# Optimization experiments

Hardware: AMD Instinct MI355X
Metric: run time of the kernel (lower is better)

The kernel has to match this reference:

```python
import jax, jax.numpy as jnp
import numpy as np
from jax import lax

D_MODEL = 1024
D_STATE = 16
D_CONV = 4
EXPAND = 2
D_INNER = EXPAND * D_MODEL            # 2048
DT_RANK = (D_MODEL + 15) // 16        # 64
B, L = 2, 2048
EPS = 1e-5


def setup_inputs() -> dict:
    key = jax.random.key(0)
    ks = jax.random.split(key, 12)
    s = 0.02
    x = jax.random.normal(ks[0], (B, L, D_MODEL), dtype=jnp.float32)
    norm_w = jnp.ones((D_MODEL,), dtype=jnp.float32)
    in_proj_w = jax.random.normal(ks[1], (2 * D_INNER, D_MODEL), dtype=jnp.float32) * s
    conv_w = jax.random.normal(ks[2], (D_INNER, D_CONV), dtype=jnp.float32) * 0.1
    conv_b = jax.random.normal(ks[3], (D_INNER,), dtype=jnp.float32) * 0.01
    x_proj_w = jax.random.normal(ks[4], (DT_RANK + 2 * D_STATE, D_INNER), dtype=jnp.float32) * s
    dt_proj_w = jax.random.normal(ks[5], (D_INNER, DT_RANK), dtype=jnp.float32) * 0.1
    dt_proj_b = jax.random.normal(ks[6], (D_INNER,), dtype=jnp.float32) * 0.5 - 4.0  # small softplus(delta)
    # S4D-real init: A = -(1..d_state) per channel
    A_log = jnp.log(jnp.broadcast_to(jnp.arange(1, D_STATE + 1, dtype=jnp.float32), (D_INNER, D_STATE)))
    Dp = jnp.ones((D_INNER,), dtype=jnp.float32)
    out_proj_w = jax.random.normal(ks[7], (D_MODEL, D_INNER), dtype=jnp.float32) * s
    return {"x": x, "norm_w": norm_w, "in_proj_w": in_proj_w, "conv_w": conv_w,
            "conv_b": conv_b, "x_proj_w": x_proj_w, "dt_proj_w": dt_proj_w,
            "dt_proj_b": dt_proj_b, "A_log": A_log, "Dp": Dp, "out_proj_w": out_proj_w}


def _selective_scan(deltaA, deltaBu, Cm):
    # deltaA, deltaBu: [B,L,Di,N]; Cm: [B,L,N] -> y: [B,L,Di]
    def step(h, inp):
        dA, dBu, c = inp
        h = dA * h + dBu                       # [B,Di,N]
        y = jnp.einsum('bdn,bn->bd', h, c)     # [B,Di]
        return h, y
    h0 = jnp.zeros(deltaA.shape[0:1] + deltaA.shape[2:], deltaA.dtype)
    _, ys = lax.scan(step, h0, (deltaA.transpose(1, 0, 2, 3),
                                deltaBu.transpose(1, 0, 2, 3),
                                Cm.transpose(1, 0, 2)))
    return ys.transpose(1, 0, 2)               # [B,L,Di]


def reference(x, norm_w, in_proj_w, conv_w, conv_b, x_proj_w,
              dt_proj_w, dt_proj_b, A_log, Dp, out_proj_w):
    d_inner, d_conv = conv_w.shape
    d_state = A_log.shape[1]
    dt_rank = dt_proj_w.shape[1]

    # RMSNorm
    rms = jnp.sqrt(jnp.mean(x * x, axis=-1, keepdims=True) + EPS)
    xn = norm_w * (x / rms)

    # input projection -> x, z streams
    xz = jnp.einsum('bld,ed->ble', xn, in_proj_w)      # [B,L,2*Di]
    xi, z = jnp.split(xz, 2, axis=-1)

    # depthwise causal conv1d + SiLU
    xc = lax.conv_general_dilated(
        xi.transpose(0, 2, 1), conv_w[:, None, :], (1,), [(d_conv - 1, 0)],
        dimension_numbers=('NCL', 'OIL', 'NCL'), feature_group_count=d_inner)
    xc = jax.nn.silu(xc.transpose(0, 2, 1) + conv_b)   # [B,L,Di]

    # input-dependent SSM params
    dbl = jnp.einsum('bld,ed->ble', xc, x_proj_w)      # [B,L,dt_rank+2N]
    dt, Bm, Cm = jnp.split(dbl, [dt_rank, dt_rank + d_state], axis=-1)
    delta = jax.nn.softplus(jnp.einsum('blr,dr->bld', dt, dt_proj_w) + dt_proj_b)

    A = -jnp.exp(A_log)                                # [Di,N]
    deltaA = jnp.exp(delta[..., None] * A)             # [B,L,Di,N]
    deltaBu = delta[..., None] * Bm[:, :, None, :] * xc[..., None]

    y = _selective_scan(deltaA, deltaBu, Cm)           # [B,L,Di]
    y = y + xc * Dp
    y = y * jax.nn.silu(z)

    out = jnp.einsum('bld,ed->ble', y, out_proj_w)     # [B,L,d_model]
    return x + out
```

## Files before the change

### kernel.cpp

```cpp
#include <hip/hip_runtime.h>
#include <hip/hip_bf16.h>
#include <math.h>

#define D_MODEL 1024
#define D_STATE 16
#define D_CONV 4
#define D_INNER 2048
#define DT_RANK 64
#define BATCH 2
#define SEQ 2048
#define NTOK (BATCH*SEQ)
#define EPS 1e-5f
#define CCH 32
#define TCH (SEQ/CCH)
#define XKS 8
#define XKC (D_INNER/XKS)

typedef __attribute__((ext_vector_type(8))) short short8;
typedef __attribute__((ext_vector_type(4))) float f32x4;
typedef __attribute__((ext_vector_type(4))) unsigned short us4;

__device__ inline unsigned short f2bf(float f) {
  union { __hip_bfloat16 h; unsigned short u; } c;
  c.h = __float2bfloat16(f);
  return c.u;
}
__device__ inline float bf2f(unsigned short u) {
  union { unsigned int i; float f; } c;
  c.i = ((unsigned int)u) << 16;
  return c.f;
}

#define GLL(gp, lp) __builtin_amdgcn_global_load_lds( \
    (const __attribute__((address_space(1))) void*)(gp), \
    (__attribute__((address_space(3))) void*)(lp), 16, 0, 0)

__global__ __launch_bounds__(256) void f2bf4_kernel(
    const float* __restrict__ i0, unsigned short* __restrict__ o0, int b0,
    const float* __restrict__ i1, unsigned short* __restrict__ o1, int b1,
    const float* __restrict__ i2, unsigned short* __restrict__ o2, int b2,
    const float* __restrict__ i3, unsigned short* __restrict__ o3)
{
  int blk = blockIdx.x;
  const float* in; unsigned short* out; int base;
  if (blk < b0)           { in = i0; out = o0; base = blk; }
  else if (blk < b0+b1)   { in = i1; out = o1; base = blk - b0; }
  else if (blk < b0+b1+b2){ in = i2; out = o2; base = blk - b0 - b1; }
  else                    { in = i3; out = o3; base = blk - b0 - b1 - b2; }
  int i = (base*256 + threadIdx.x)*4;
  float4 v = *(const float4*)(in + i);
  us4 o;
  o[0] = f2bf(v.x); o[1] = f2bf(v.y); o[2] = f2bf(v.z); o[3] = f2bf(v.w);
  *(us4*)(out + i) = o;
}

__global__ __launch_bounds__(256) void rmsnorm_kernel(const float* __restrict__ x,
                                                      const float* __restrict__ w,
                                                      unsigned short* __restrict__ xn) {
  int tok = blockIdx.x;
  const float* xr = x + (size_t)tok * D_MODEL;
  unsigned short* xo = xn + (size_t)tok * D_MODEL;
  int t = threadIdx.x;
  float4 v = ((const float4*)xr)[t];
  float ss = v.x*v.x + v.y*v.y + v.z*v.z + v.w*v.w;
  #pragma unroll
  for (int off = 32; off > 0; off >>= 1) ss += __shfl_down(ss, off, 64);
  __shared__ float wsum[4];
  __shared__ float rinv_s;
  int lane = t & 63, wv = t >> 6;
  if (lane == 0) wsum[wv] = ss;
  __syncthreads();
  if (t == 0) {
    float tot = wsum[0] + wsum[1] + wsum[2] + wsum[3];
    rinv_s = 1.0f / sqrtf(tot / (float)D_MODEL + EPS);
  }
  __syncthreads();
  float rinv = rinv_s;
  float4 g = ((const float4*)w)[t];
  us4 o;
  o[0] = f2bf(v.x * rinv * g.x);
  o[1] = f2bf(v.y * rinv * g.y);
  o[2] = f2bf(v.z * rinv * g.z);
  o[3] = f2bf(v.w * rinv * g.w);
  *(us4*)(xo + t*4) = o;
}

template<int EPI, int OBF>
__global__ __launch_bounds__(256) void gemm_bf16_kernel(
    const unsigned short* __restrict__ A,
    const unsigned short* __restrict__ W,
    void* __restrict__ Cv, int ldc, int K,
    const float* __restrict__ bias,
    const float* __restrict__ resid)
{
  __shared__ __align__(16) unsigned short Abuf[8*64*8];
  __shared__ __align__(16) unsigned short Bbuf[8*64*8];
  int tid = threadIdx.x;
  int lane = tid & 63;
  int w = tid >> 6;
  int bm = blockIdx.x * 128;
  int bn = blockIdx.y * 128;
  int wrow = (w >> 1) * 64;
  int wcol = (w & 1) * 64;

  int r15 = lane & 15, g = lane >> 4;
  const unsigned short* Ag0 = A + (size_t)(bm + 2*w*16 + r15) * K + g*8;
  const unsigned short* Ag1 = Ag0 + (size_t)16 * K;
  const unsigned short* Wg0 = W + (size_t)(bn + 2*w*16 + r15) * K + g*8;
  const unsigned short* Wg1 = Wg0 + (size_t)16 * K;
  unsigned short* Al0 = &Abuf[(2*w  )*512];
  unsigned short* Al1 = &Abuf[(2*w+1)*512];
  unsigned short* Bl0 = &Bbuf[(2*w  )*512];
  unsigned short* Bl1 = &Bbuf[(2*w+1)*512];

  f32x4 acc[4][4] = {};

  for (int k0 = 0; k0 < K; k0 += 32) {
    __syncthreads();
    GLL(Ag0 + k0, Al0);
    GLL(Ag1 + k0, Al1);
    GLL(Wg0 + k0, Bl0);
    GLL(Wg1 + k0, Bl1);
    __syncthreads();

    short8 af[4], bfr[4];
    #pragma unroll
    for (int i = 0; i < 4; ++i)
      af[i] = *(const short8*)&Abuf[((wrow >> 4) + i)*512 + lane*8];
    #pragma unroll
    for (int j = 0; j < 4; ++j)
      bfr[j] = *(const short8*)&Bbuf[((wcol >> 4) + j)*512 + lane*8];
    #pragma unroll
    for (int i = 0; i < 4; ++i)
      #pragma unroll
      for (int j = 0; j < 4; ++j)
        acc[i][j] = __builtin_amdgcn_mfma_f32_16x16x32_bf16(af[i], bfr[j], acc[i][j], 0, 0, 0);
  }

  #pragma unroll
  for (int i = 0; i < 4; ++i) {
    #pragma unroll
    for (int j = 0; j < 4; ++j) {
      #pragma unroll
      for (int r = 0; r < 4; ++r) {
        int row = bm + wrow + i*16 + (lane >> 4)*4 + r;
        int col = bn + wcol + j*16 + (lane & 15);
        float v = acc[i][j][r];
        if (EPI == 1) {
          float s = v + bias[col];
          v = fmaxf(s, 0.f) + log1pf(__expf(-fabsf(s)));
        } else if (EPI == 2) {
          v += resid[(size_t)row * ldc + col];
        }
        if (OBF) ((unsigned short*)Cv)[(size_t)row * ldc + col] = f2bf(v);
        else     ((float*)Cv)[(size_t)row * ldc + col] = v;
      }
    }
  }
}

__global__ __launch_bounds__(256) void xproj_bf16_kernel(
    const unsigned short* __restrict__ A,
    const unsigned short* __restrict__ W,
    float* __restrict__ Ppart)
{
  __shared__ __align__(16) unsigned short Abuf[8*512];
  __shared__ __align__(16) unsigned short Bbuf[6*512];
  int tid = threadIdx.x;
  int lane = tid & 63;
  int w = tid >> 6;
  int bm = blockIdx.x * 128;
  int kc = blockIdx.y;
  const int K = D_INNER;
  int r15 = lane & 15, g = lane >> 4;

  const unsigned short* Ag0 = A + (size_t)(bm + 2*w*16 + r15) * K + g*8 + kc*XKC;
  const unsigned short* Ag1 = Ag0 + (size_t)16 * K;
  const unsigned short* Wg0 = W + (size_t)(w*16 + r15) * K + g*8 + kc*XKC;
  const unsigned short* Wg1 = W + (size_t)((4+w)*16 + r15) * K + g*8 + kc*XKC;
  unsigned short* Al0 = &Abuf[(2*w  )*512];
  unsigned short* Al1 = &Abuf[(2*w+1)*512];
  unsigned short* Bl0 = &Bbuf[w*512];
  unsigned short* Bl1 = &Bbuf[(4+w)*512];

  f32x4 acc[2][6] = {};

  for (int k0 = 0; k0 < XKC; k0 += 32) {
    __syncthreads();
    GLL(Ag0 + k0, Al0);
    GLL(Ag1 + k0, Al1);
    GLL(Wg0 + k0, Bl0);
    if (w < 2) GLL(Wg1 + k0, Bl1);
    __syncthreads();

    short8 af[2], bfr[6];
    #pragma unroll
    for (int i = 0; i < 2; ++i)
      af[i] = *(const short8*)&Abuf[(2*w + i)*512 + lane*8];
    #pragma unroll
    for (int j = 0; j < 6; ++j)
      bfr[j] = *(const short8*)&Bbuf[j*512 + lane*8];
    #pragma unroll
    for (int i = 0; i < 2; ++i)
      #pragma unroll
      for (int j = 0; j < 6; ++j)
        acc[i][j] = __builtin_amdgcn_mfma_f32_16x16x32_bf16(af[i], bfr[j], acc[i][j], 0, 0, 0);
  }

  float* out = Ppart + (size_t)kc * NTOK * 96;
  #pragma unroll
  for (int i = 0; i < 2; ++i) {
    #pragma unroll
    for (int j = 0; j < 6; ++j) {
      #pragma unroll
      for (int r = 0; r < 4; ++r) {
        int row = bm + w*32 + i*16 + (lane >> 4)*4 + r;
        int col = j*16 + (lane & 15);
        out[(size_t)row * 96 + col] = acc[i][j][r];
      }
    }
  }
}

__global__ __launch_bounds__(256) void xproj_reduce_kernel(
    const float* __restrict__ Ppart, float* __restrict__ dbl,
    unsigned short* __restrict__ dtbf)
{
  int idx = blockIdx.x * 256 + threadIdx.x;
  float s = 0.f;
  #pragma unroll
  for (int k = 0; k < XKS; ++k) s += Ppart[(size_t)k * NTOK * 96 + idx];
  dbl[idx] = s;
  int row = idx / 96, col = idx - row * 96;
  if (col < DT_RANK) dtbf[(size_t)row * DT_RANK + col] = f2bf(s);
}

__global__ __launch_bounds__(256) void conv_silu_kernel(
    const unsigned short* __restrict__ xz, const float* __restrict__ cw,
    const float* __restrict__ cb, unsigned short* __restrict__ xcbf)
{
  int idx = blockIdx.x * 256 + threadIdx.x;
  int dq = idx & (D_INNER/4 - 1);
  int tok = idx >> 9;
  int l = tok & (SEQ - 1);
  int d = dq * 4;
  const unsigned short* xi = xz + (size_t)tok * (2*D_INNER) + d;
  us4 v3 = *(const us4*)xi;
  us4 v2 = l >= 1 ? *(const us4*)(xi - 1*(2*D_INNER)) : (us4)0;
  us4 v1 = l >= 2 ? *(const us4*)(xi - 2*(2*D_INNER)) : (us4)0;
  us4 v0 = l >= 3 ? *(const us4*)(xi - 3*(2*D_INNER)) : (us4)0;
  float4 cbv = *(const float4*)(cb + d);
  float cbx[4] = {cbv.x, cbv.y, cbv.z, cbv.w};
  us4 o;
  #pragma unroll
  for (int j = 0; j < 4; ++j) {
    float4 wv = *(const float4*)(cw + (d + j) * 4);
    float s = cbx[j];
    s = fmaf(bf2f(v0[j]), wv.x, s);
    s = fmaf(bf2f(v1[j]), wv.y, s);
    s = fmaf(bf2f(v2[j]), wv.z, s);
    s = fmaf(bf2f(v3[j]), wv.w, s);
    float v = s / (1.f + __expf(-s));
    o[j] = f2bf(v);
  }
  *(us4*)(xcbf + (size_t)tok * D_INNER + d) = o;
}

__global__ __launch_bounds__(256) void scan_pass1(
    const unsigned short* __restrict__ delta, const float* __restrict__ dbl,
    const unsigned short* __restrict__ xc, const float* __restrict__ A_log,
    float* __restrict__ P, float* __restrict__ He)
{
  int blk = blockIdx.x;
  int d = (blk & 7) * 256 + threadIdx.x;
  int c = (blk >> 3) & (CCH - 1);
  int b = blk >> 8;
  float Adn[16];
  #pragma unroll
  for (int n = 0; n < 16; ++n) Adn[n] = -__expf(A_log[d*16 + n]);
  float h[16] = {};
  float sdl = 0.f;
  int tok0 = b * SEQ + c * TCH;
  for (int t = 0; t < TCH; ++t) {
    size_t tok = (size_t)(tok0 + t);
    float dl = bf2f(delta[tok * D_INNER + d]);
    float xcv = bf2f(xc[tok * D_INNER + d]);
    float u = dl * xcv;
    const float4* bp = (const float4*)(dbl + tok*96 + 64);
    float4 b0 = bp[0], b1 = bp[1], b2 = bp[2], b3 = bp[3];
    float bv[16] = {b0.x,b0.y,b0.z,b0.w, b1.x,b1.y,b1.z,b1.w,
                    b2.x,b2.y,b2.z,b2.w, b3.x,b3.y,b3.z,b3.w};
    sdl += dl;
    #pragma unroll
    for (int n = 0; n < 16; ++n)
      h[n] = fmaf(__expf(dl * Adn[n]), h[n], u * bv[n]);
  }
  size_t base = ((size_t)(b*CCH + c) * 16) * D_INNER + d;
  #pragma unroll
  for (int n = 0; n < 16; ++n) {
    P [base + (size_t)n * D_INNER] = __expf(Adn[n] * sdl);
    He[base + (size_t)n * D_INNER] = h[n];
  }
}

__global__ __launch_bounds__(256) void scan_pass2(
    const float* __restrict__ P, const float* __restrict__ He,
    float* __restrict__ Hin)
{
  int blk = blockIdx.x;
  int d = (blk & 7) * 256 + threadIdx.x;
  int n = (blk >> 3) & 15;
  int b = blk >> 7;
  float h = 0.f;
  #pragma unroll 4
  for (int c = 0; c < CCH; ++c) {
    size_t idx = ((size_t)(b*CCH + c) * 16 + n) * D_INNER + d;
    Hin[idx] = h;
    h = fmaf(P[idx], h, He[idx]);
  }
}

__global__ __launch_bounds__(256) void scan_pass3(
    const unsigned short* __restrict__ delta, const float* __restrict__ dbl,
    const unsigned short* __restrict__ xc, const unsigned short* __restrict__ xz,
    const float* __restrict__ A_log, const float* __restrict__ Dp,
    const float* __restrict__ Hin, unsigned short* __restrict__ y)
{
  int blk = blockIdx.x;
  int d = (blk & 7) * 256 + threadIdx.x;
  int c = (blk >> 3) & (CCH - 1);
  int b = blk >> 8;
  float Adn[16];
  #pragma unroll
  for (int n = 0; n < 16; ++n) Adn[n] = -__expf(A_log[d*16 + n]);
  float Dpd = Dp[d];
  float h[16];
  size_t base = ((size_t)(b*CCH + c) * 16) * D_INNER + d;
  #pragma unroll
  for (int n = 0; n < 16; ++n) h[n] = Hin[base + (size_t)n * D_INNER];
  int tok0 = b * SEQ + c * TCH;
  for (int t = 0; t < TCH; ++t) {
    size_t tok = (size_t)(tok0 + t);
    float dl = bf2f(delta[tok * D_INNER + d]);
    float xcv = bf2f(xc[tok * D_INNER + d]);
    float u = dl * xcv;
    const float4* bp = (const float4*)(dbl + tok*96 + 64);
    float4 b0 = bp[0], b1 = bp[1], b2 = bp[2], b3 = bp[3];
    float4 c0 = bp[4], c1 = bp[5], c2 = bp[6], c3 = bp[7];
    float bv[16] = {b0.x,b0.y,b0.z,b0.w, b1.x,b1.y,b1.z,b1.w,
                    b2.x,b2.y,b2.z,b2.w, b3.x,b3.y,b3.z,b3.w};
    float cv[16] = {c0.x,c0.y,c0.z,c0.w, c1.x,c1.y,c1.z,c1.w,
                    c2.x,c2.y,c2.z,c2.w, c3.x,c3.y,c3.z,c3.w};
    float z = bf2f(xz[tok * (2*D_INNER) + D_INNER + d]);
    float acc = xcv * Dpd;
    #pragma unroll
    for (int n = 0; n < 16; ++n) {
      h[n] = fmaf(__expf(dl * Adn[n]), h[n], u * bv[n]);
      acc = fmaf(h[n], cv[n], acc);
    }
    float sz = z / (1.f + __expf(-z));
    y[tok * D_INNER + d] = f2bf(acc * sz);
  }
}

extern "C" void kernel_launch(void* const* d_in, const int* in_sizes, int n_in,
                              void* d_out, int out_size, void* d_ws, size_t ws_size,
                              hipStream_t stream) {
  const float* x         = (const float*)d_in[0];
  const float* norm_w    = (const float*)d_in[1];
  const float* in_proj_w = (const float*)d_in[2];
  const float* conv_w    = (const float*)d_in[3];
  const float* conv_b    = (const float*)d_in[4];
  const float* x_proj_w  = (const float*)d_in[5];
  const float* dt_proj_w = (const float*)d_in[6];
  const float* dt_proj_b = (const float*)d_in[7];
  const float* A_log     = (const float*)d_in[8];
  const float* Dp        = (const float*)d_in[9];
  const float* out_proj_w= (const float*)d_in[10];
  float* out = (float*)d_out;

  char* ws = (char*)d_ws;
  unsigned short* xz_bf   = (unsigned short*)(ws);
  unsigned short* xc_bf   = (unsigned short*)(ws + ( 32ull<<20));
  float*          dbl     = (float*)(ws + ( 48ull<<20));
  unsigned short* delta_bf= (unsigned short*)(ws + ( 50ull<<20));
  unsigned short* xn_bf   = (unsigned short*)(ws + ( 66ull<<20));
  unsigned short* w_in_bf = (unsigned short*)(ws + ( 74ull<<20));
  unsigned short* w_out_bf= (unsigned short*)(ws + ( 82ull<<20));
  unsigned short* w_xp_bf = (unsigned short*)(ws + ( 86ull<<20));
  unsigned short* w_dt_bf = (unsigned short*)(ws + ( 87ull<<20));
  unsigned short* dtbf    = (unsigned short*)(ws + ( 88ull<<20));
  float*          Ppart   = (float*)(ws + ( 89ull<<20));
  float*          Pst     = (float*)(ws + (102ull<<20));
  float*          Hest    = (float*)(ws + (110ull<<20));
  float*          Hin     = (float*)(ws + (118ull<<20));
  unsigned short* yb_bf   = (unsigned short*)(ws + (126ull<<20));

  rmsnorm_kernel<<<NTOK, 256, 0, stream>>>(x, norm_w, xn_bf);

  f2bf4_kernel<<<4096+2048+192+128, 256, 0, stream>>>(
      in_proj_w, w_in_bf, 4096,
      out_proj_w, w_out_bf, 2048,
      x_proj_w, w_xp_bf, 192,
      dt_proj_w, w_dt_bf);

  {
    dim3 g(NTOK/128, (2*D_INNER)/128);
    gemm_bf16_kernel<0,1><<<g, 256, 0, stream>>>(xn_bf, w_in_bf, xz_bf, 2*D_INNER, D_MODEL,
                                                 nullptr, nullptr);
  }

  conv_silu_kernel<<<(NTOK*D_INNER/4)/256, 256, 0, stream>>>(xz_bf, conv_w, conv_b, xc_bf);

  {
    dim3 g(NTOK/128, XKS);
    xproj_bf16_kernel<<<g, 256, 0, stream>>>(xc_bf, w_xp_bf, Ppart);
    xproj_reduce_kernel<<<(NTOK*96)/256, 256, 0, stream>>>(Ppart, dbl, dtbf);
  }

  {
    dim3 g(NTOK/128, D_INNER/128);
    gemm_bf16_kernel<1,1><<<g, 256, 0, stream>>>(dtbf, w_dt_bf, delta_bf, D_INNER, DT_RANK,
                                                 dt_proj_b, nullptr);
  }

  scan_pass1<<<BATCH*CCH*8, 256, 0, stream>>>(delta_bf, dbl, xc_bf, A_log, Pst, Hest);
  scan_pass2<<<BATCH*16*8, 256, 0, stream>>>(Pst, Hest, Hin);
  scan_pass3<<<BATCH*CCH*8, 256, 0, stream>>>(delta_bf, dbl, xc_bf, xz_bf, A_log, Dp, Hin, yb_bf);

  {
    dim3 g(NTOK/128, D_MODEL/128);
    gemm_bf16_kernel<2,0><<<g, 256, 0, stream>>>(yb_bf, w_out_bf, out, D_MODEL, D_INNER,
                                                 nullptr, x);
  }
}
```

Before: 385.3 us.

## Add 256x256 double-buffered MFMA GEMM kernel for in_proj

Replaces the 128x128 tile GEMM for the input projection with a new 512-thread kernel using 256x256 tiles. It loads global memory directly into LDS with double buffering and runs a four-phase software pipeline that interleaves MFMA with staged loads, controlled by explicit waitcnt, barriers and priority hints. The larger tiles raise data reuse per byte loaded. In exchange the grid shrinks to 256 blocks, LDS use rises to 128KB per block, and register pressure goes up, which limits occupancy.

```diff
diff --git a/kernel.cpp b/kernel.cpp
--- a/kernel.cpp
+++ b/kernel.cpp
@@ -83,6 +83,125 @@
   o[2] = f2bf(v.z * rinv * g.z);
   o[3] = f2bf(v.w * rinv * g.w);
   *(us4*)(xo + t*4) = o;
+}
+
+template<int NT>
+__global__ __launch_bounds__(512) void gemm256_bf16_kernel(
+    const unsigned short* __restrict__ A,
+    const unsigned short* __restrict__ W,
+    unsigned short* __restrict__ C, int ldc)
+{
+  const int K = NT*64;
+  __shared__ __align__(16) unsigned short As[2][16384];
+  __shared__ __align__(16) unsigned short Bs[2][16384];
+  int tid = threadIdx.x;
+  int lane = tid & 63;
+  int w = tid >> 6;
+  int wm = w >> 2, wn = w & 3;
+  int bm = blockIdx.x * 256;
+  int bn = blockIdx.y * 256;
+  int r15 = lane & 15, g8 = (lane >> 4) * 8;
+  int rbh0 = (w & 3) + (w >> 2) * 8;
+  int rbh1 = rbh0 + 4;
+
+  auto stageA = [&](int slot, int tile, int ks, int rb) {
+    const unsigned short* src = A + (size_t)(bm + rb*16 + r15) * K + tile*64 + ks*32 + g8;
+    GLL(src, &As[slot][rb*1024 + ks*512]);
+  };
+  auto stageB = [&](int slot, int tile, int ks, int cb) {
+    const unsigned short* src = W + (size_t)(bn + cb*16 + r15) * K + tile*64 + ks*32 + g8;
+    GLL(src, &Bs[slot][cb*1024 + ks*512]);
+  };
+
+  stageA(0,0,0,rbh0); stageB(0,0,0,w); stageB(0,0,0,8+w);
+  stageA(0,0,0,rbh1);
+  stageA(0,0,1,rbh0); stageB(0,0,1,w); stageB(0,0,1,8+w);
+  stageA(0,0,1,rbh1);
+  stageA(1,1,0,rbh0); stageB(1,1,0,w); stageB(1,1,0,8+w);
+  stageA(1,1,0,rbh1);
+  stageA(1,1,1,rbh0); stageB(1,1,1,w); stageB(1,1,1,8+w);
+  asm volatile("s_waitcnt vmcnt(7)" ::: "memory");
+  __builtin_amdgcn_s_barrier();
+  __builtin_amdgcn_sched_barrier(0);
+
+  f32x4 acc[8][4] = {};
+  short8 bfr[4];
+
+#define PHASE_END()                                                      \
+  if (drain) { asm volatile("s_waitcnt vmcnt(0)" ::: "memory"); }        \
+  else       { asm volatile("s_waitcnt vmcnt(12)" ::: "memory"); }       \
+  __builtin_amdgcn_s_barrier();                                          \
+  __builtin_amdgcn_sched_barrier(0);
+
+#define MFMA16(IH)                                                       \
+  __builtin_amdgcn_s_setprio(1);                                         \
+  _Pragma("unroll")                                                      \
+  for (int ii = 0; ii < 4; ++ii) {                                       \
+    _Pragma("unroll")                                                    \
+    for (int j = 0; j < 4; ++j)                                          \
+      acc[(IH)*4+ii][j] = __builtin_amdgcn_mfma_f32_16x16x32_bf16(       \
+          af[ii], bfr[j], acc[(IH)*4+ii][j], 0, 0, 0);                   \
+  }                                                                      \
+  __builtin_amdgcn_s_setprio(0);
+
+#define LOAD_A(KS, IH)                                                   \
+  short8 af[4];                                                          \
+  _Pragma("unroll")                                                      \
+  for (int ii = 0; ii < 4; ++ii)                                         \
+    af[ii] = *(const short8*)&As[s][(wm*8 + (IH)*4 + ii)*1024 + (KS)*512 + lane*8];
+
+#define LOAD_B(KS)                                                       \
+  _Pragma("unroll")                                                      \
+  for (int j = 0; j < 4; ++j)                                            \
+    bfr[j] = *(const short8*)&Bs[s][(wn*4 + j)*1024 + (KS)*512 + lane*8];
+
+  for (int t = 0; t < NT; ++t) {
+    int s = t & 1;
+    const bool drain = (t >= NT-2);
+    {
+      LOAD_A(0,0)
+      LOAD_B(0)
+      if (t+1 < NT) { stageA(s^1, t+1, 1, rbh1); }
+      MFMA16(0)
+      PHASE_END()
+    }
+    {
+      LOAD_A(0,1)
+      if (t+2 < NT) { stageA(s, t+2, 0, rbh0); stageB(s, t+2, 0, w); stageB(s, t+2, 0, 8+w); }
+      MFMA16(1)
+      PHASE_END()
+    }
+    {
+      LOAD_A(1,0)
+      LOAD_B(1)
+      if (t+2 < NT) { stageA(s, t+2, 0, rbh1); }
+      MFMA16(0)
+      PHASE_END()
+    }
+    {
+      LOAD_A(1,1)
+      if (t+2 < NT) { stageA(s, t+2, 1, rbh0); stageB(s, t+2, 1, w); stageB(s, t+2, 1, 8+w); }
+      MFMA16(1)
+      PHASE_END()
+    }
+  }
+#undef PHASE_END
+#undef MFMA16
+#undef LOAD_A
+#undef LOAD_B
+
+  #pragma unroll
+  for (int ig = 0; ig < 8; ++ig) {
+    #pragma unroll
+    for (int j = 0; j < 4; ++j) {
+      #pragma unroll
+      for (int r = 0; r < 4; ++r) {
+        int row = bm + wm*128 + ig*16 + (lane >> 4)*4 + r;
+        int col = bn + wn*64 + j*16 + r15;
+        C[(size_t)row * ldc + col] = f2bf(acc[ig][j][r]);
+      }
+    }
+  }
 }
 
 template<int EPI, int OBF>
@@ -405,9 +524,8 @@
       dt_proj_w, w_dt_bf);
 
   {
-    dim3 g(NTOK/128, (2*D_INNER)/128);
-    gemm_bf16_kernel<0,1><<<g, 256, 0, stream>>>(xn_bf, w_in_bf, xz_bf, 2*D_INNER, D_MODEL,
-                                                 nullptr, nullptr);
+    dim3 g(NTOK/256, (2*D_INNER)/256);
+    gemm256_bf16_kernel<D_MODEL/64><<<g, 512, 0, stream>>>(xn_bf, w_in_bf, xz_bf, 2*D_INNER);
   }
 
   conv_silu_kernel<<<(NTOK*D_INNER/4)/256, 256, 0, stream>>>(xz_bf, conv_w, conv_b, xc_bf);
```

New measurement: 350.6 us. -9.0%, faster.
